# Optimization experiments

Measured on AMD Instinct MI355X. Metric: run time of the kernel, lower is better.

The kernel has to match this reference:

```python
import jax, jax.numpy as jnp
import numpy as np

N_DATA = 1200000
FEAT = 128
BATCH = 512
N_NEG = 4096
TEMP = 0.07
MOMENTUM = 0.5


def _l2norm(x):
    return x / jnp.maximum(jnp.linalg.norm(x, axis=-1, keepdims=True), 1e-12)


def setup_inputs() -> dict:
    key = jax.random.key(0)
    k1, k2, k3, k4, k5 = jax.random.split(key, 5)
    negatives = _l2norm(jax.random.normal(k1, (N_DATA, FEAT), dtype=jnp.float32))
    return {
        "student_feat": jax.random.normal(k2, (BATCH, FEAT), dtype=jnp.float32),
        "teacher_feat": jax.random.normal(k3, (BATCH, FEAT), dtype=jnp.float32),
        "negatives": negatives,
        "indices": jax.random.randint(k4, (BATCH,), 0, N_DATA, dtype=jnp.int64)
            if jax.config.read("jax_enable_x64") else jax.random.randint(k4, (BATCH,), 0, N_DATA, dtype=jnp.int32),
        "neg_indices": jax.random.randint(k5, (BATCH, N_NEG), 0, N_DATA, dtype=jnp.int32),
    }


def reference(student_feat, teacher_feat, negatives, indices, neg_indices):
    s = _l2norm(student_feat)                       # [B, D]
    t = _l2norm(teacher_feat)                       # [B, D]
    pos_sim = jnp.sum(s * t, axis=1) / TEMP         # [B]
    neg_feat = negatives[neg_indices]               # [B, K, D] gather from bank
    neg_sim = jnp.einsum('bd,bkd->bk', s, neg_feat) / TEMP  # [B, K]
    logits = jnp.concatenate([pos_sim[:, None], neg_sim], axis=1)  # [B, 1+K]
    # cross-entropy with label 0 for every row
    loss = jnp.mean(jax.nn.logsumexp(logits, axis=1) - logits[:, 0])
    # EMA scatter update + renormalize of touched rows (no-grad side effect)
    upd = MOMENTUM * negatives[indices] + (1.0 - MOMENTUM) * t
    upd = _l2norm(upd)
    new_negatives = negatives.at[indices].set(upd)
    return loss, new_negatives
```

## Files before the change

kernel.cpp:

```cpp
#include <hip/hip_runtime.h>

constexpr int   FEAT   = 128;
constexpr int   BATCH  = 512;
constexpr int   NNEG   = 4096;
constexpr long  NDATA  = 1200000;
constexpr int   CHUNKS = 8;
constexpr int   NCOPY  = 1024;
constexpr float INV_TEMP = 14.285714285714286f;
constexpr float LOG2E    = 1.4426950408889634f;
constexpr float LN2      = 0.6931471805599453f;
constexpr float K1       = INV_TEMP * LOG2E;

typedef float f4 __attribute__((ext_vector_type(4)));

__global__ __launch_bounds__(128) void prep_kernel(
    const float* __restrict__ sf, const float* __restrict__ tf,
    float* __restrict__ s_n, float* __restrict__ t_n, float* __restrict__ pos) {
  const int b = blockIdx.x, t = threadIdx.x;
  const float sv = sf[b * FEAT + t];
  const float tv = tf[b * FEAT + t];
  float ss = sv * sv, tt = tv * tv, st = sv * tv;
#pragma unroll
  for (int m = 1; m < 64; m <<= 1) {
    ss += __shfl_xor(ss, m);
    tt += __shfl_xor(tt, m);
    st += __shfl_xor(st, m);
  }
  __shared__ float sh[6];
  if ((t & 63) == 0) {
    const int w = t >> 6;
    sh[w * 3 + 0] = ss; sh[w * 3 + 1] = tt; sh[w * 3 + 2] = st;
  }
  __syncthreads();
  ss = sh[0] + sh[3]; tt = sh[1] + sh[4]; st = sh[2] + sh[5];
  const float snorm = fmaxf(sqrtf(ss), 1e-12f);
  const float tnorm = fmaxf(sqrtf(tt), 1e-12f);
  s_n[b * FEAT + t] = sv / snorm;
  t_n[b * FEAT + t] = tv / tnorm;
  if (t == 0) pos[b] = st / (snorm * tnorm) * INV_TEMP;
}

__global__ __launch_bounds__(256) void work_kernel(
    const float* __restrict__ neg, const int* __restrict__ nidx,
    const float* __restrict__ s_n, float* __restrict__ sumexp,
    float* __restrict__ dst) {
  __shared__ float part[4];
  if (blockIdx.x < NCOPY) {
    const long n4 = NDATA * (long)FEAT / 4;
    long i = (long)blockIdx.x * blockDim.x + threadIdx.x;
    const long stride = (long)NCOPY * blockDim.x;
    for (; i < n4; i += stride) {
      const f4 v = *((const f4*)neg + i);
      float* d = dst + 4 * i;
      __builtin_nontemporal_store(v.x, d + 0);
      __builtin_nontemporal_store(v.y, d + 1);
      __builtin_nontemporal_store(v.z, d + 2);
      __builtin_nontemporal_store(v.w, d + 3);
    }
    return;
  }
  const int blk   = blockIdx.x - NCOPY;
  const int b     = blk >> 3;
  const int chunk = blk & (CHUNKS - 1);
  const int lane  = threadIdx.x & 63;
  const int w     = threadIdx.x >> 6;
  const float2 s2 = *(const float2*)(s_n + b * FEAT + 2 * lane);
  constexpr int KPC = NNEG / CHUNKS;
  constexpr int KPW = KPC / 4;
  const int* row_idx = nidx + b * NNEG + chunk * KPC + w * KPW;
  float acc = 0.f;
  for (int k = 0; k < KPW; k += 8) {
    int   idx[8];
    float p[8];
#pragma unroll
    for (int u = 0; u < 8; ++u) idx[u] = row_idx[k + u];
    float2 nv[8];
#pragma unroll
    for (int u = 0; u < 8; ++u)
      nv[u] = *(const float2*)(neg + (long)idx[u] * FEAT + 2 * lane);
#pragma unroll
    for (int u = 0; u < 8; ++u) p[u] = fmaf(s2.x, nv[u].x, s2.y * nv[u].y);
#pragma unroll
    for (int m = 1; m < 64; m <<= 1) {
#pragma unroll
      for (int u = 0; u < 8; ++u) p[u] += __shfl_xor(p[u], m);
    }
#pragma unroll
    for (int u = 0; u < 8; ++u) acc += exp2f(fmaf(p[u], K1, -K1));
  }
  if (lane == 0) part[w] = acc;
  __syncthreads();
  if (threadIdx.x == 0)
    sumexp[b * CHUNKS + chunk] = part[0] + part[1] + part[2] + part[3];
}

__global__ __launch_bounds__(256) void finish_kernel(
    const float* __restrict__ pos, const float* __restrict__ sumexp,
    const float* __restrict__ neg, const float* __restrict__ t_n,
    const int* __restrict__ indices, float* __restrict__ out) {
  const int t = threadIdx.x;
  if (blockIdx.x == 0) {
    float lsum = 0.f;
#pragma unroll
    for (int r = t; r < BATCH; r += 256) {
      const float p = pos[r];
      float tot = exp2f(fmaf(p, LOG2E, -K1));
#pragma unroll
      for (int c = 0; c < CHUNKS; ++c) tot += sumexp[r * CHUNKS + c];
      lsum += INV_TEMP + log2f(tot) * LN2 - p;
    }
#pragma unroll
    for (int m = 1; m < 64; m <<= 1) lsum += __shfl_xor(lsum, m);
    __shared__ float sh[4];
    if ((t & 63) == 0) sh[t >> 6] = lsum;
    __syncthreads();
    if (t == 0) out[0] = (sh[0] + sh[1] + sh[2] + sh[3]) / (float)BATCH;
    return;
  }
  const int b = blockIdx.x - 1;
  float* dst = out + 1;
  __shared__ int sidx[BATCH];
  __shared__ int flag;
  if (t == 0) flag = 0;
  for (int j = t; j < BATCH; j += 256) sidx[j] = indices[j];
  __syncthreads();
  const int idx = sidx[b];
  int later = 0;
  for (int j = t; j < BATCH; j += 256)
    if (j > b && sidx[j] == idx) later = 1;
  if (later) flag = 1;
  __syncthreads();
  if (flag) return;
  float u = 0.f, uu = 0.f;
  if (t < FEAT) {
    u = 0.5f * neg[(long)idx * FEAT + t] + 0.5f * t_n[b * FEAT + t];
    uu = u * u;
  }
#pragma unroll
  for (int m = 1; m < 64; m <<= 1) uu += __shfl_xor(uu, m);
  __shared__ float sh2[2];
  if (t == 0 || t == 64) sh2[t >> 6] = uu;
  __syncthreads();
  if (t < FEAT) {
    const float nrm = fmaxf(sqrtf(sh2[0] + sh2[1]), 1e-12f);
    dst[(long)idx * FEAT + t] = u / nrm;
  }
}

extern "C" void kernel_launch(void* const* d_in, const int* in_sizes, int n_in,
                              void* d_out, int out_size, void* d_ws, size_t ws_size,
                              hipStream_t stream) {
  const float* student   = (const float*)d_in[0];
  const float* teacher   = (const float*)d_in[1];
  const float* negatives = (const float*)d_in[2];
  const int*   indices   = (const int*)d_in[3];
  const int*   neg_idx   = (const int*)d_in[4];
  float* out = (float*)d_out;

  float* ws     = (float*)d_ws;
  float* s_n    = ws;
  float* t_n    = s_n + BATCH * FEAT;
  float* pos    = t_n + BATCH * FEAT;
  float* sumexp = pos + BATCH;

  prep_kernel<<<BATCH, 128, 0, stream>>>(student, teacher, s_n, t_n, pos);
  work_kernel<<<NCOPY + BATCH * CHUNKS, 256, 0, stream>>>(
      negatives, neg_idx, s_n, sumexp, out + 1);
  finish_kernel<<<1 + BATCH, 256, 0, stream>>>(
      pos, sumexp, negatives, t_n, indices, out);
}
```

Baseline: 397.5 us.

## Compute negative dot products one row per thread instead of per wavefront

Restructures the gather-dot stage so each thread loads two whole negative rows with 16-byte vector loads and dots them against the student vector staged in LDS. This replaces the wavefront-wide float2 loads and the butterfly shuffle reduction per row. The goal is to remove most cross-lane shuffle work and per-row overhead. The cost is that each load instruction now touches 64 scattered cache lines, which relies on L1/L2 to absorb the strided per-thread access.

```diff
diff --git a/kernel.cpp b/kernel.cpp
--- a/kernel.cpp
+++ b/kernel.cpp
@@ -44,7 +44,6 @@
     const float* __restrict__ neg, const int* __restrict__ nidx,
     const float* __restrict__ s_n, float* __restrict__ sumexp,
     float* __restrict__ dst) {
-  __shared__ float part[4];
   if (blockIdx.x < NCOPY) {
     const long n4 = NDATA * (long)FEAT / 4;
     long i = (long)blockIdx.x * blockDim.x + threadIdx.x;
@@ -59,39 +58,36 @@
     }
     return;
   }
+  __shared__ float s_lds[FEAT];
+  __shared__ float part[4];
   const int blk   = blockIdx.x - NCOPY;
   const int b     = blk >> 3;
   const int chunk = blk & (CHUNKS - 1);
-  const int lane  = threadIdx.x & 63;
-  const int w     = threadIdx.x >> 6;
-  const float2 s2 = *(const float2*)(s_n + b * FEAT + 2 * lane);
-  constexpr int KPC = NNEG / CHUNKS;
-  constexpr int KPW = KPC / 4;
-  const int* row_idx = nidx + b * NNEG + chunk * KPC + w * KPW;
-  float acc = 0.f;
-  for (int k = 0; k < KPW; k += 8) {
-    int   idx[8];
-    float p[8];
+  const int t     = threadIdx.x;
+  if (t < FEAT) s_lds[t] = s_n[b * FEAT + t];
+  __syncthreads();
+  const int kbase = b * NNEG + chunk * (NNEG / CHUNKS) + t;
+  const long i0 = (long)nidx[kbase] * FEAT;
+  const long i1 = (long)nidx[kbase + 256] * FEAT;
+  f4 a0 = {0.f, 0.f, 0.f, 0.f};
+  f4 a1 = {0.f, 0.f, 0.f, 0.f};
 #pragma unroll
-    for (int u = 0; u < 8; ++u) idx[u] = row_idx[k + u];
-    float2 nv[8];
+  for (int f = 0; f < FEAT; f += 4) {
+    const f4 sv = *(const f4*)(s_lds + f);
+    const f4 r0 = *(const f4*)(neg + i0 + f);
+    const f4 r1 = *(const f4*)(neg + i1 + f);
+    a0 += sv * r0;
+    a1 += sv * r1;
+  }
+  const float d0 = (a0.x + a0.y) + (a0.z + a0.w);
+  const float d1 = (a1.x + a1.y) + (a1.z + a1.w);
+  float term = exp2f(fmaf(d0, K1, -K1)) + exp2f(fmaf(d1, K1, -K1));
 #pragma unroll
-    for (int u = 0; u < 8; ++u)
-      nv[u] = *(const float2*)(neg + (long)idx[u] * FEAT + 2 * lane);
-#pragma unroll
-    for (int u = 0; u < 8; ++u) p[u] = fmaf(s2.x, nv[u].x, s2.y * nv[u].y);
-#pragma unroll
-    for (int m = 1; m < 64; m <<= 1) {
-#pragma unroll
-      for (int u = 0; u < 8; ++u) p[u] += __shfl_xor(p[u], m);
-    }
-#pragma unroll
-    for (int u = 0; u < 8; ++u) acc += exp2f(fmaf(p[u], K1, -K1));
-  }
-  if (lane == 0) part[w] = acc;
+  for (int m = 1; m < 64; m <<= 1) term += __shfl_xor(term, m);
+  if ((t & 63) == 0) part[t >> 6] = term;
   __syncthreads();
-  if (threadIdx.x == 0)
-    sumexp[b * CHUNKS + chunk] = part[0] + part[1] + part[2] + part[3];
+  if (t == 0)
+    sumexp[blk] = part[0] + part[1] + part[2] + part[3];
 }
 
 __global__ __launch_bounds__(256) void finish_kernel(
```

Measured after the change: 537.5 us. +35.2%, slower.
